# Optimization experiments

Hardware: AMD Instinct MI355X
Metric: run time of the kernel (lower is better)

The kernel has to match this reference:

```python
import jax, jax.numpy as jnp
import numpy as np

SR = 16000
N_WT = 10
WT_LEN = 512
FIR_TAPS = 31
NU_C = 0.1
N_REFLECT = (FIR_TAPS - 1) // 2
B, L = 16, 160000


def setup_inputs() -> dict:
    key = jax.random.key(0)
    k1, k2, k3, k4 = jax.random.split(key, 4)
    # F0 in a realistic [100, 400) Hz range
    pitch = jax.random.uniform(k1, (B, L, 1), jnp.float32) * 300.0 + 100.0
    envelope = jax.random.uniform(k2, (B, L, 1), jnp.float32)
    # attention weights are 'already softmaxed' over the wavetable axis
    attention = jax.nn.softmax(jax.random.normal(k3, (B, L, N_WT), jnp.float32), axis=-1)
    # learned wavetables, init N(0, 0.01) as in the torch module (n_pure_harmonics=0)
    wavetables = jax.random.normal(k4, (N_WT, WT_LEN), jnp.float32) * 0.01
    # fixed windowed-sinc low-pass FIR (Type I), same construction as __init__
    n = np.arange(-(FIR_TAPS - 1) // 2, 1 + (FIR_TAPS - 1) // 2, dtype=np.float32)
    h = 2.0 * NU_C * np.sinc(2.0 * NU_C * n) * np.hamming(FIR_TAPS)
    fir_h = jnp.asarray(h, jnp.float32)
    return {"pitch": pitch, "envelope": envelope, "attention": attention,
            "wavetables": wavetables, "fir_h": fir_h}


def reference(pitch, envelope, attention, wavetables, fir_h):
    # circular ('reflect' in the repo's naming) pad each wavetable: (W, 512+2*15)
    wt_pad = jnp.concatenate(
        [wavetables[:, -N_REFLECT:], wavetables, wavetables[:, :N_REFLECT]], axis=1)
    # torch conv1d is cross-correlation; jnp.correlate 'valid' matches -> (W, 512)
    wt = jax.vmap(lambda x: jnp.correlate(x, fir_h, mode='valid'))(wt_pad)

    L_wt = WT_LEN
    freqs = pitch[..., 0]                       # (B, L)
    increment = (L_wt / SR) * freqs             # phase increment per sample
    # NOTE: faithful to torch code: increment[0] is the FIRST BATCH ROW (L,)
    index = jnp.cumsum(increment, axis=1) - increment[0]
    index = jnp.remainder(index, L_wt)
    index = jnp.where(L_wt - index < 1e-5, 0.0, index)
    idx_lo_f = jnp.floor(index)
    alpha = index - idx_lo_f                    # (B, L)
    i_lo = idx_lo_f.astype(jnp.int32)
    i_hi = jnp.ceil(index).astype(jnp.int32) % L_wt

    # gather all wavetables at once: (W, B, L)
    lo = jnp.take(wt, i_lo, axis=1)
    hi = jnp.take(wt, i_hi, axis=1)
    wave = lo + alpha[None, :, :] * (hi - lo)   # linear interpolation
    wave = jnp.transpose(wave, (1, 2, 0))       # (B, L, W)

    out = jnp.sum(wave * attention, axis=2, keepdims=True) * envelope  # (B, L, 1)
    return out
```

## Files before the change

### kernel.cpp

```cpp
#include <hip/hip_runtime.h>

#define N_WT_     10
#define WT_LEN_   512
#define FIR_TAPS_ 31
#define N_REFL_   15
#define B_        16
#define L_        160000

constexpr int   TPB   = 256;
constexpr int   TPS   = 1024;
constexpr float INCF  = 0.032f;
constexpr int   NG0   = L_ / 16;
constexpr int   NG1   = NG0 / 16;
constexpr int   NG2   = 40;
constexpr int   NG3   = 3;

__global__ __launch_bounds__(TPB) void ysum_kernel(
        const float* __restrict__ pitch, float* __restrict__ y,
        const float* __restrict__ wavetables, const float* __restrict__ fir_h,
        float* __restrict__ wt2) {
    __shared__ float s_pad[WT_LEN_ + 2 * N_REFL_];
    __shared__ float s_h[FIR_TAPS_];
    const int b = blockIdx.y, bx = blockIdx.x, t = threadIdx.x;

    const bool do_fir = (b == 0) && (bx < N_WT_);
    if (do_fir) {
        if (t < FIR_TAPS_) s_h[t] = fir_h[t];
        for (int j = t; j < WT_LEN_ + 2 * N_REFL_; j += TPB) {
            int src = (j + WT_LEN_ - N_REFL_) % WT_LEN_;
            s_pad[j] = wavetables[bx * WT_LEN_ + src];
        }
        __syncthreads();
        for (int i = t; i < WT_LEN_; i += TPB) {
            float acc = 0.0f;
#pragma unroll
            for (int tap = 0; tap < FIR_TAPS_; ++tap)
                acc = fmaf(s_h[tap], s_pad[i + tap], acc);
            wt2[i * N_WT_ + bx] = acc;
            if (i == 0) wt2[WT_LEN_ * N_WT_ + bx] = acc;
        }
    }

    const int g = bx * 256 + t;
    if (g < NG0) {
        const float4* p4 = (const float4*)(pitch + (size_t)b * L_ + (size_t)g * 16);
        float4 v0 = p4[0], v1 = p4[1], v2 = p4[2], v3 = p4[3];
        float xs[16] = {v0.x, v0.y, v0.z, v0.w, v1.x, v1.y, v1.z, v1.w,
                        v2.x, v2.y, v2.z, v2.w, v3.x, v3.y, v3.z, v3.w};
        float acc = 0.0f;
#pragma unroll
        for (int i = 0; i < 16; ++i) {
            float inc = INCF * xs[i];
            asm("" : "+v"(inc));
            acc += inc;
        }
        y[b * NG0 + g] = acc;
    }
}

__global__ __launch_bounds__(TPS) void scan_kernel(
        const float* __restrict__ y, float* __restrict__ S1) {
    __shared__ __align__(16) float s_y[NG0];
    __shared__ __align__(16) float s_S1[NG0];
    __shared__ float s_z[NG1];
    __shared__ float s_S2[NG1];
    __shared__ float s_w[NG2], s_S3[NG2];
    __shared__ float s_v[NG3], s_S4[NG3];
    const int b = blockIdx.x, t = threadIdx.x;
    const float* yrow = y + (size_t)b * NG0;
    {
        const float2* src = (const float2*)yrow;
        float2* dst = (float2*)s_y;
        for (int i = t; i < NG0 / 2; i += TPS) dst[i] = src[i];
    }
    __syncthreads();
    for (int j = t; j < NG1; j += TPS) {
        float a = 0.0f;
        for (int i = 0; i < 16; ++i) a += s_y[16 * j + i];
        s_z[j] = a;
    }
    __syncthreads();
    if (t < NG2) {
        float a = 0.0f;
        int hi = min(16 * t + 16, NG1);
        for (int i = 16 * t; i < hi; ++i) a += s_z[i];
        s_w[t] = a;
    }
    __syncthreads();
    if (t < NG3) {
        float a = 0.0f;
        int hi = min(16 * t + 16, NG2);
        for (int i = 16 * t; i < hi; ++i) a += s_w[i];
        s_v[t] = a;
    }
    __syncthreads();
    if (t == 0) {
        float run = 0.0f;
        for (int m = 0; m < NG3; ++m) { run += s_v[m]; s_S4[m] = run; }
    }
    __syncthreads();
    if (t < NG2) {
        float a = 0.0f;
        for (int i = (t >> 4) << 4; i <= t; ++i) a += s_w[i];
        if (t >= 16) a = a + s_S4[(t >> 4) - 1];
        s_S3[t] = a;
    }
    __syncthreads();
    if (t < NG2) {
        float r = 0.0f;
        float carry = (t > 0) ? s_S3[t - 1] : 0.0f;
        int hi = min(16 * t + 16, NG1);
        for (int k = 16 * t; k < hi; ++k) {
            r += s_z[k];
            s_S2[k] = (t > 0) ? r + carry : r;
        }
    }
    __syncthreads();
    for (int j = t; j < NG1; j += TPS) {
        float r = 0.0f;
        float carry = (j > 0) ? s_S2[j - 1] : 0.0f;
        for (int k = 0; k < 16; ++k) {
            r += s_y[16 * j + k];
            s_S1[16 * j + k] = (j > 0) ? r + carry : r;
        }
    }
    __syncthreads();
    float* S1row = S1 + (size_t)b * NG0;
    {
        const float2* src = (const float2*)s_S1;
        float2* dst = (float2*)S1row;
        for (int i = t; i < NG0 / 2; i += TPS) dst[i] = src[i];
    }
}

__global__ __launch_bounds__(TPB) void synth_kernel(
        const float* __restrict__ pitch,
        const float* __restrict__ envelope,
        const float* __restrict__ attention,
        const float* __restrict__ wt2,
        const float* __restrict__ S1,
        float* __restrict__ out) {
    const int b = blockIdx.y, cb = blockIdx.x, t = threadIdx.x;
    const int    l = cb * TPB + t;
    const size_t g = (size_t)b * L_ + l;

    const float pv  = pitch[g];
    const float p0  = pitch[l];
    const float env = envelope[g];
    const int   g0  = l >> 4;
    const float carry = (g0 > 0) ? S1[(size_t)b * NG0 + g0 - 1] : 0.0f;
    const float2* ap = (const float2*)(attention + g * (size_t)N_WT_);
    float2 a01 = ap[0], a23 = ap[1], a45 = ap[2], a67 = ap[3], a89 = ap[4];

    const int lane  = t & 63;
    const int r16   = lane & 15;
    const int sbase = lane & ~15;

    float x = INCF * pv;
    float acc = 0.0f;
#pragma unroll
    for (int k = 0; k < 16; ++k) {
        float v = __shfl(x, sbase + k, 64);
        acc += (k <= r16) ? v : 0.0f;
    }
    if (g0 > 0) acc = acc + carry;

    float idx = acc - INCF * p0;
    float r = fmodf(idx, 512.0f);
    if (r < 0.0f) r += 512.0f;
    if (512.0f - r < 1e-5f) r = 0.0f;
    float fl = floorf(r);
    float alpha = r - fl;
    int lo = (int)fl;

    const float2* pw = (const float2*)(wt2 + lo * N_WT_);
    float2 q0 = pw[0], q1 = pw[1], q2 = pw[2], q3 = pw[3], q4 = pw[4];
    float2 q5 = pw[5], q6 = pw[6], q7 = pw[7], q8 = pw[8], q9 = pw[9];
    float loV[10] = {q0.x, q0.y, q1.x, q1.y, q2.x, q2.y, q3.x, q3.y, q4.x, q4.y};
    float hiV[10] = {q5.x, q5.y, q6.x, q6.y, q7.x, q7.y, q8.x, q8.y, q9.x, q9.y};
    float a[10] = {a01.x, a01.y, a23.x, a23.y, a45.x, a45.y,
                   a67.x, a67.y, a89.x, a89.y};

    float a0 = 0.0f;
#pragma unroll
    for (int w = 0; w < N_WT_; ++w)
        a0 += a[w] * (loV[w] + alpha * (hiV[w] - loV[w]));
    out[g] = a0 * env;
}

extern "C" void kernel_launch(void* const* d_in, const int* in_sizes, int n_in,
                              void* d_out, int out_size, void* d_ws, size_t ws_size,
                              hipStream_t stream) {
    const float* pitch      = (const float*)d_in[0];
    const float* envelope   = (const float*)d_in[1];
    const float* attention  = (const float*)d_in[2];
    const float* wavetables = (const float*)d_in[3];
    const float* fir_h      = (const float*)d_in[4];
    float*       out        = (float*)d_out;

    char*  ws  = (char*)d_ws;
    float* wt2 = (float*)(ws);
    float* y   = (float*)(ws + 32768);
    float* S1  = (float*)(ws + 32768 + 655360);

    ysum_kernel<<<dim3(40, B_), dim3(TPB), 0, stream>>>(
        pitch, y, wavetables, fir_h, wt2);
    scan_kernel<<<dim3(B_), dim3(TPS), 0, stream>>>(y, S1);
    synth_kernel<<<dim3(NG1, B_), dim3(TPB), 0, stream>>>(
        pitch, envelope, attention, wt2, S1, out);
}
```

Baseline: 187.2 us.

## Restructure hierarchical scan so synth reconstructs level-1 prefixes from y and S2

Moves the level-2 partial sums into the ysum kernel using wavefront shuffles. The scan kernel now only scans the small z array with 128 threads, where before it loaded and wrote the full 10000-element S1 row per batch. The synth kernel rebuilds each 16-sample group's carry from y and S2 with an extra shuffle reduction. The wavetable is repacked with lo and hi values interleaved in 20-float rows so each lookup uses float4 loads. This shortens the serial single-block-per-batch scan stage at the cost of extra shuffles and loads in synth.

```diff
diff --git a/kernel.cpp b/kernel.cpp
--- a/kernel.cpp
+++ b/kernel.cpp
@@ -8,17 +8,19 @@
 #define L_        160000
 
 constexpr int   TPB   = 256;
-constexpr int   TPS   = 1024;
+constexpr int   TSC   = 128;
 constexpr float INCF  = 0.032f;
 constexpr int   NG0   = L_ / 16;
 constexpr int   NG1   = NG0 / 16;
 constexpr int   NG2   = 40;
 constexpr int   NG3   = 3;
+constexpr int   WROW  = 20;
 
 __global__ __launch_bounds__(TPB) void ysum_kernel(
         const float* __restrict__ pitch, float* __restrict__ y,
+        float* __restrict__ z,
         const float* __restrict__ wavetables, const float* __restrict__ fir_h,
-        float* __restrict__ wt2) {
+        float* __restrict__ wt3) {
     __shared__ float s_pad[WT_LEN_ + 2 * N_REFL_];
     __shared__ float s_h[FIR_TAPS_];
     const int b = blockIdx.y, bx = blockIdx.x, t = threadIdx.x;
@@ -36,18 +38,19 @@
 #pragma unroll
             for (int tap = 0; tap < FIR_TAPS_; ++tap)
                 acc = fmaf(s_h[tap], s_pad[i + tap], acc);
-            wt2[i * N_WT_ + bx] = acc;
-            if (i == 0) wt2[WT_LEN_ * N_WT_ + bx] = acc;
+            wt3[i * WROW + bx] = acc;
+            wt3[((i + 511) & 511) * WROW + 10 + bx] = acc;
         }
     }
 
     const int g = bx * 256 + t;
-    if (g < NG0) {
+    const bool valid = (g < NG0);
+    float acc = 0.0f;
+    if (valid) {
         const float4* p4 = (const float4*)(pitch + (size_t)b * L_ + (size_t)g * 16);
         float4 v0 = p4[0], v1 = p4[1], v2 = p4[2], v3 = p4[3];
         float xs[16] = {v0.x, v0.y, v0.z, v0.w, v1.x, v1.y, v1.z, v1.w,
                         v2.x, v2.y, v2.z, v2.w, v3.x, v3.y, v3.z, v3.w};
-        float acc = 0.0f;
 #pragma unroll
         for (int i = 0; i < 16; ++i) {
             float inc = INCF * xs[i];
@@ -56,29 +59,26 @@
         }
         y[b * NG0 + g] = acc;
     }
-}
-
-__global__ __launch_bounds__(TPS) void scan_kernel(
-        const float* __restrict__ y, float* __restrict__ S1) {
-    __shared__ __align__(16) float s_y[NG0];
-    __shared__ __align__(16) float s_S1[NG0];
+
+    const int lane = t & 63, r16 = lane & 15, sbase = lane & ~15;
+    float zacc = 0.0f;
+#pragma unroll
+    for (int k = 0; k < 16; ++k) {
+        float v = __shfl(acc, sbase + k, 64);
+        zacc += v;
+    }
+    if (r16 == 15 && valid) z[b * NG1 + (g >> 4)] = zacc;
+}
+
+__global__ __launch_bounds__(TSC) void scan_kernel(
+        const float* __restrict__ z, float* __restrict__ S2) {
     __shared__ float s_z[NG1];
     __shared__ float s_S2[NG1];
     __shared__ float s_w[NG2], s_S3[NG2];
     __shared__ float s_v[NG3], s_S4[NG3];
     const int b = blockIdx.x, t = threadIdx.x;
-    const float* yrow = y + (size_t)b * NG0;
-    {
-        const float2* src = (const float2*)yrow;
-        float2* dst = (float2*)s_y;
-        for (int i = t; i < NG0 / 2; i += TPS) dst[i] = src[i];
-    }
-    __syncthreads();
-    for (int j = t; j < NG1; j += TPS) {
-        float a = 0.0f;
-        for (int i = 0; i < 16; ++i) a += s_y[16 * j + i];
-        s_z[j] = a;
-    }
+    const float* zrow = z + (size_t)b * NG1;
+    for (int i = t; i < NG1; i += TSC) s_z[i] = zrow[i];
     __syncthreads();
     if (t < NG2) {
         float a = 0.0f;
@@ -116,45 +116,37 @@
         }
     }
     __syncthreads();
-    for (int j = t; j < NG1; j += TPS) {
-        float r = 0.0f;
-        float carry = (j > 0) ? s_S2[j - 1] : 0.0f;
-        for (int k = 0; k < 16; ++k) {
-            r += s_y[16 * j + k];
-            s_S1[16 * j + k] = (j > 0) ? r + carry : r;
-        }
-    }
-    __syncthreads();
-    float* S1row = S1 + (size_t)b * NG0;
-    {
-        const float2* src = (const float2*)s_S1;
-        float2* dst = (float2*)S1row;
-        for (int i = t; i < NG0 / 2; i += TPS) dst[i] = src[i];
-    }
+    float* S2row = S2 + (size_t)b * NG1;
+    for (int i = t; i < NG1; i += TSC) S2row[i] = s_S2[i];
 }
 
 __global__ __launch_bounds__(TPB) void synth_kernel(
         const float* __restrict__ pitch,
         const float* __restrict__ envelope,
         const float* __restrict__ attention,
-        const float* __restrict__ wt2,
-        const float* __restrict__ S1,
+        const float* __restrict__ wt3,
+        const float* __restrict__ y,
+        const float* __restrict__ S2,
         float* __restrict__ out) {
     const int b = blockIdx.y, cb = blockIdx.x, t = threadIdx.x;
     const int    l = cb * TPB + t;
     const size_t g = (size_t)b * L_ + l;
 
+    const int lane  = t & 63;
+    const int r16   = lane & 15;
+    const int sbase = lane & ~15;
+    const int jj    = t >> 4;
+
     const float pv  = pitch[g];
     const float p0  = pitch[l];
     const float env = envelope[g];
-    const int   g0  = l >> 4;
-    const float carry = (g0 > 0) ? S1[(size_t)b * NG0 + g0 - 1] : 0.0f;
+    const float* yrow = y + (size_t)b * NG0;
+    const float yown  = yrow[16 * cb + r16];
+    const float yprev = (cb > 0) ? yrow[16 * cb - 16 + r16] : 0.0f;
+    const int   ci    = cb - 1 - (jj == 0 ? 1 : 0);
+    const float s2v   = (ci >= 0) ? S2[(size_t)b * NG1 + ci] : 0.0f;
     const float2* ap = (const float2*)(attention + g * (size_t)N_WT_);
     float2 a01 = ap[0], a23 = ap[1], a45 = ap[2], a67 = ap[3], a89 = ap[4];
-
-    const int lane  = t & 63;
-    const int r16   = lane & 15;
-    const int sbase = lane & ~15;
 
     float x = INCF * pv;
     float acc = 0.0f;
@@ -163,7 +155,19 @@
         float v = __shfl(x, sbase + k, 64);
         acc += (k <= r16) ? v : 0.0f;
     }
-    if (g0 > 0) acc = acc + carry;
+
+    const float ysel = (jj == 0) ? yprev : yown;
+    const int   n    = (jj == 0) ? 16 : jj;
+    float rr = 0.0f;
+#pragma unroll
+    for (int k = 0; k < 16; ++k) {
+        float v = __shfl(ysel, sbase + k, 64);
+        rr += (k < n) ? v : 0.0f;
+    }
+    if (!(cb == 0 && jj == 0)) {
+        float S1prev = (ci >= 0) ? (rr + s2v) : rr;
+        acc = acc + S1prev;
+    }
 
     float idx = acc - INCF * p0;
     float r = fmodf(idx, 512.0f);
@@ -173,11 +177,10 @@
     float alpha = r - fl;
     int lo = (int)fl;
 
-    const float2* pw = (const float2*)(wt2 + lo * N_WT_);
-    float2 q0 = pw[0], q1 = pw[1], q2 = pw[2], q3 = pw[3], q4 = pw[4];
-    float2 q5 = pw[5], q6 = pw[6], q7 = pw[7], q8 = pw[8], q9 = pw[9];
-    float loV[10] = {q0.x, q0.y, q1.x, q1.y, q2.x, q2.y, q3.x, q3.y, q4.x, q4.y};
-    float hiV[10] = {q5.x, q5.y, q6.x, q6.y, q7.x, q7.y, q8.x, q8.y, q9.x, q9.y};
+    const float4* pw = (const float4*)(wt3 + lo * WROW);
+    float4 q0 = pw[0], q1 = pw[1], q2 = pw[2], q3 = pw[3], q4 = pw[4];
+    float loV[10] = {q0.x, q0.y, q0.z, q0.w, q1.x, q1.y, q1.z, q1.w, q2.x, q2.y};
+    float hiV[10] = {q2.z, q2.w, q3.x, q3.y, q3.z, q3.w, q4.x, q4.y, q4.z, q4.w};
     float a[10] = {a01.x, a01.y, a23.x, a23.y, a45.x, a45.y,
                    a67.x, a67.y, a89.x, a89.y};
 
@@ -199,13 +202,14 @@
     float*       out        = (float*)d_out;
 
     char*  ws  = (char*)d_ws;
-    float* wt2 = (float*)(ws);
-    float* y   = (float*)(ws + 32768);
-    float* S1  = (float*)(ws + 32768 + 655360);
+    float* wt3 = (float*)(ws);
+    float* y   = (float*)(ws + 40960);
+    float* z   = (float*)(ws + 40960 + 640000);
+    float* S2  = (float*)(ws + 40960 + 640000 + 40000);
 
     ysum_kernel<<<dim3(40, B_), dim3(TPB), 0, stream>>>(
-        pitch, y, wavetables, fir_h, wt2);
-    scan_kernel<<<dim3(B_), dim3(TPS), 0, stream>>>(y, S1);
+        pitch, y, z, wavetables, fir_h, wt3);
+    scan_kernel<<<dim3(B_), dim3(TSC), 0, stream>>>(z, S2);
     synth_kernel<<<dim3(NG1, B_), dim3(TPB), 0, stream>>>(
-        pitch, envelope, attention, wt2, S1, out);
-}
+        pitch, envelope, attention, wt3, y, S2, out);
+}
```

Result: no change. 189.9 us (+1.5%).

## Stage wavetable in LDS and process five chunks per block with prefetch

Applied to the files above, without the earlier changes.

The synth kernel now copies the filtered wavetable (about 20 KB) into shared memory once per block and gathers from LDS instead of global or L2. Each block handles five 256-sample chunks and prefetches the next chunk's inputs in software while computing the current one, which cuts the grid by five. The aim is to lower gather latency and overlap the streaming loads. In exchange, every block pays for the table copy plus a barrier, uses more registers, and has fewer blocks available for latency hiding.

```diff
diff --git a/kernel.cpp b/kernel.cpp
--- a/kernel.cpp
+++ b/kernel.cpp
@@ -14,6 +14,8 @@
 constexpr int   NG1   = NG0 / 16;
 constexpr int   NG2   = 40;
 constexpr int   NG3   = 3;
+constexpr int   CPB   = 5;
+constexpr int   WTI   = (WT_LEN_ + 1) * N_WT_;
 
 __global__ __launch_bounds__(TPB) void ysum_kernel(
         const float* __restrict__ pitch, float* __restrict__ y,
@@ -133,6 +135,26 @@
     }
 }
 
+struct SIn {
+    float  pv, p0, env, carry;
+    float2 a0, a1, a2, a3, a4;
+};
+
+__device__ __forceinline__ SIn load_in(int l, size_t rowb,
+        const float* __restrict__ pitch, const float* __restrict__ envelope,
+        const float* __restrict__ attention, const float* __restrict__ S1row) {
+    SIn s;
+    const size_t g = rowb + l;
+    s.pv  = pitch[g];
+    s.p0  = pitch[l];
+    s.env = envelope[g];
+    const int g0 = l >> 4;
+    s.carry = (g0 > 0) ? S1row[g0 - 1] : 0.0f;
+    const float2* ap = (const float2*)(attention + g * (size_t)N_WT_);
+    s.a0 = ap[0]; s.a1 = ap[1]; s.a2 = ap[2]; s.a3 = ap[3]; s.a4 = ap[4];
+    return s;
+}
+
 __global__ __launch_bounds__(TPB) void synth_kernel(
         const float* __restrict__ pitch,
         const float* __restrict__ envelope,
@@ -140,52 +162,67 @@
         const float* __restrict__ wt2,
         const float* __restrict__ S1,
         float* __restrict__ out) {
+    __shared__ __align__(8) float s_wt[WTI];
     const int b = blockIdx.y, cb = blockIdx.x, t = threadIdx.x;
-    const int    l = cb * TPB + t;
-    const size_t g = (size_t)b * L_ + l;
-
-    const float pv  = pitch[g];
-    const float p0  = pitch[l];
-    const float env = envelope[g];
-    const int   g0  = l >> 4;
-    const float carry = (g0 > 0) ? S1[(size_t)b * NG0 + g0 - 1] : 0.0f;
-    const float2* ap = (const float2*)(attention + g * (size_t)N_WT_);
-    float2 a01 = ap[0], a23 = ap[1], a45 = ap[2], a67 = ap[3], a89 = ap[4];
+    const size_t rowb = (size_t)b * L_;
+    const float* S1row = S1 + (size_t)b * NG0;
+    const int l0 = cb * (TPB * CPB) + t;
+
+    SIn cur = load_in(l0, rowb, pitch, envelope, attention, S1row);
+
+    {
+        const float2* src = (const float2*)wt2;
+        float2* dst = (float2*)s_wt;
+        for (int i = t; i < WTI / 2; i += TPB) dst[i] = src[i];
+    }
+    __syncthreads();
 
     const int lane  = t & 63;
     const int r16   = lane & 15;
     const int sbase = lane & ~15;
 
-    float x = INCF * pv;
-    float acc = 0.0f;
-#pragma unroll
-    for (int k = 0; k < 16; ++k) {
-        float v = __shfl(x, sbase + k, 64);
-        acc += (k <= r16) ? v : 0.0f;
-    }
-    if (g0 > 0) acc = acc + carry;
-
-    float idx = acc - INCF * p0;
-    float r = fmodf(idx, 512.0f);
-    if (r < 0.0f) r += 512.0f;
-    if (512.0f - r < 1e-5f) r = 0.0f;
-    float fl = floorf(r);
-    float alpha = r - fl;
-    int lo = (int)fl;
-
-    const float2* pw = (const float2*)(wt2 + lo * N_WT_);
-    float2 q0 = pw[0], q1 = pw[1], q2 = pw[2], q3 = pw[3], q4 = pw[4];
-    float2 q5 = pw[5], q6 = pw[6], q7 = pw[7], q8 = pw[8], q9 = pw[9];
-    float loV[10] = {q0.x, q0.y, q1.x, q1.y, q2.x, q2.y, q3.x, q3.y, q4.x, q4.y};
-    float hiV[10] = {q5.x, q5.y, q6.x, q6.y, q7.x, q7.y, q8.x, q8.y, q9.x, q9.y};
-    float a[10] = {a01.x, a01.y, a23.x, a23.y, a45.x, a45.y,
-                   a67.x, a67.y, a89.x, a89.y};
-
-    float a0 = 0.0f;
-#pragma unroll
-    for (int w = 0; w < N_WT_; ++w)
-        a0 += a[w] * (loV[w] + alpha * (hiV[w] - loV[w]));
-    out[g] = a0 * env;
+#pragma unroll
+    for (int cc = 0; cc < CPB; ++cc) {
+        SIn nxt = cur;
+        if (cc + 1 < CPB)
+            nxt = load_in(l0 + (cc + 1) * TPB, rowb, pitch, envelope,
+                          attention, S1row);
+        const int l = l0 + cc * TPB;
+
+        float x = INCF * cur.pv;
+        float acc = 0.0f;
+#pragma unroll
+        for (int k = 0; k < 16; ++k) {
+            float v = __shfl(x, sbase + k, 64);
+            acc += (k <= r16) ? v : 0.0f;
+        }
+        const int g0 = l >> 4;
+        if (g0 > 0) acc = acc + cur.carry;
+
+        float idx = acc - INCF * cur.p0;
+        float r = fmodf(idx, 512.0f);
+        if (r < 0.0f) r += 512.0f;
+        if (512.0f - r < 1e-5f) r = 0.0f;
+        float fl = floorf(r);
+        float alpha = r - fl;
+        int lo = (int)fl;
+
+        const float2* pw = (const float2*)(s_wt + lo * N_WT_);
+        float2 q0 = pw[0], q1 = pw[1], q2 = pw[2], q3 = pw[3], q4 = pw[4];
+        float2 q5 = pw[5], q6 = pw[6], q7 = pw[7], q8 = pw[8], q9 = pw[9];
+        float loV[10] = {q0.x, q0.y, q1.x, q1.y, q2.x, q2.y, q3.x, q3.y, q4.x, q4.y};
+        float hiV[10] = {q5.x, q5.y, q6.x, q6.y, q7.x, q7.y, q8.x, q8.y, q9.x, q9.y};
+        float a[10] = {cur.a0.x, cur.a0.y, cur.a1.x, cur.a1.y, cur.a2.x,
+                       cur.a2.y, cur.a3.x, cur.a3.y, cur.a4.x, cur.a4.y};
+
+        float a0 = 0.0f;
+#pragma unroll
+        for (int w = 0; w < N_WT_; ++w)
+            a0 += a[w] * (loV[w] + alpha * (hiV[w] - loV[w]));
+        out[rowb + l] = a0 * cur.env;
+
+        cur = nxt;
+    }
 }
 
 extern "C" void kernel_launch(void* const* d_in, const int* in_sizes, int n_in,
@@ -206,6 +243,6 @@
     ysum_kernel<<<dim3(40, B_), dim3(TPB), 0, stream>>>(
         pitch, y, wavetables, fir_h, wt2);
     scan_kernel<<<dim3(B_), dim3(TPS), 0, stream>>>(y, S1);
-    synth_kernel<<<dim3(NG1, B_), dim3(TPB), 0, stream>>>(
+    synth_kernel<<<dim3(L_ / (TPB * CPB), B_), dim3(TPB), 0, stream>>>(
         pitch, envelope, attention, wt2, S1, out);
 }
```

After: 190.1 us. No clear change (+1.6%).
